# Kernel tuning notes

Measured on AMD Instinct MI355X. Metric: run time of the kernel, lower is better.

Reference implementation:

```python
import jax, jax.numpy as jnp
import numpy as np

EPS = 1e-5


def setup_inputs() -> dict:
    key = jax.random.key(0)
    ks = jax.random.split(key, 4)
    b, c, h, w = 4, 256, 64, 64
    x = jax.random.normal(ks[0], (b, c, h, w), dtype=jnp.float32)
    W_qkv = jax.random.normal(ks[1], (3 * c, c), dtype=jnp.float32) * (1.0 / np.sqrt(c))
    b_qkv = jnp.zeros((3 * c,), dtype=jnp.float32)
    W_out = jax.random.normal(ks[2], (c, c), dtype=jnp.float32) * (1.0 / np.sqrt(c))
    b_out = jnp.zeros((c,), dtype=jnp.float32)
    gamma = jnp.ones((c,), dtype=jnp.float32)
    beta = jnp.zeros((c,), dtype=jnp.float32)
    return {"x": x, "W_qkv": W_qkv, "b_qkv": b_qkv, "W_out": W_out,
            "b_out": b_out, "gamma": gamma, "beta": beta}


def reference(x, W_qkv, b_qkv, W_out, b_out, gamma, beta):
    b, c, h, w = x.shape
    n = h * w  # number of spatial tokens

    # BatchNorm2d (training mode: batch statistics over b,h,w per channel)
    mean = jnp.mean(x, axis=(0, 2, 3), keepdims=True)
    var = jnp.var(x, axis=(0, 2, 3), keepdims=True)
    x_norm = (x - mean) * jax.lax.rsqrt(var + EPS)
    x_norm = x_norm * gamma[None, :, None, None] + beta[None, :, None, None]

    # 1x1 conv to QKV: [b, 3c, h, w]
    qkv = jnp.einsum('bchw,oc->bohw', x_norm, W_qkv) + b_qkv[None, :, None, None]
    q, k, v = jnp.split(qkv, 3, axis=1)

    q = q.transpose(0, 2, 3, 1).reshape(b, n, c)  # [b, n, c]
    k = k.reshape(b, c, n)                         # [b, c, n]
    v = v.transpose(0, 2, 3, 1).reshape(b, n, c)  # [b, n, c]

    scale = c ** (-0.5)
    dot = jnp.einsum('bqc,bck->bqk', q, k) * scale  # [b, n, n]
    attn = jax.nn.softmax(dot, axis=-1)
    out = jnp.einsum('bqk,bkc->bqc', attn, v)       # [b, n, c]
    out = out.reshape(b, h, w, c).transpose(0, 3, 1, 2)  # [b, c, h, w]

    # 1x1 output conv + residual
    out = jnp.einsum('bchw,oc->bohw', out, W_out) + b_out[None, :, None, None]
    return out + x
```

## Files before the change

kernel.cpp:

```cpp
#include <hip/hip_runtime.h>
#include <hip/hip_bf16.h>

typedef __attribute__((ext_vector_type(4))) float f32x4;
typedef __attribute__((ext_vector_type(8))) short bf16x8;
typedef __attribute__((ext_vector_type(4))) unsigned int u32x4;

#define BB 4
#define C 256
#define N 4096
#define TS 32
#define EPSI 1e-5f

__device__ __forceinline__ unsigned short f2bf(float f) {
    unsigned int u = __builtin_bit_cast(unsigned int, f);
    u += 0x7fffu + ((u >> 16) & 1u);
    return (unsigned short)(u >> 16);
}

__device__ __forceinline__ float bf2f(unsigned short h) {
    unsigned int u = ((unsigned int)h) << 16;
    return __builtin_bit_cast(float, u);
}

__device__ __forceinline__ unsigned int cvt_pk_bf16(float lo, float hi) {
    unsigned int r;
    asm("v_cvt_pk_bf16_f32 %0, %1, %2" : "=v"(r) : "v"(lo), "v"(hi));
    return r;
}

__device__ __forceinline__ void stage16(const unsigned short* g, unsigned short* l) {
    __builtin_amdgcn_global_load_lds(
        (const __attribute__((address_space(1))) void*)g,
        (__attribute__((address_space(3))) void*)l, 16, 0, 0);
}

__global__ __launch_bounds__(256) void bn_stats_k(
    const float* __restrict__ x, const float* __restrict__ gamma,
    const float* __restrict__ beta, float* __restrict__ scale, float* __restrict__ shift)
{
    int c = blockIdx.x;
    int tid = threadIdx.x;
    float s = 0.f, s2 = 0.f;
    for (int b = 0; b < BB; ++b) {
        const float4* p = (const float4*)(x + ((size_t)b * C + c) * N);
        for (int i = tid; i < N / 4; i += 256) {
            float4 v = p[i];
            s  += v.x + v.y + v.z + v.w;
            s2 += v.x * v.x + v.y * v.y + v.z * v.z + v.w * v.w;
        }
    }
    for (int m = 1; m < 64; m <<= 1) {
        s  += __shfl_xor(s, m);
        s2 += __shfl_xor(s2, m);
    }
    __shared__ float rs[4], rs2[4];
    int w = tid >> 6;
    if ((tid & 63) == 0) { rs[w] = s; rs2[w] = s2; }
    __syncthreads();
    if (tid == 0) {
        float S  = rs[0] + rs[1] + rs[2] + rs[3];
        float S2 = rs2[0] + rs2[1] + rs2[2] + rs2[3];
        const float inv_n = 1.f / (BB * N);
        float mean = S * inv_n;
        float var  = S2 * inv_n - mean * mean;
        float sc = gamma[c] * rsqrtf(var + EPSI);
        scale[c] = sc;
        shift[c] = beta[c] - mean * sc;
    }
}

__global__ __launch_bounds__(256) void qkv_gemm_k(
    const float* __restrict__ x, const float* __restrict__ Wqkv, const float* __restrict__ bqkv,
    const float* __restrict__ scale, const float* __restrict__ shift,
    unsigned short* __restrict__ q, unsigned short* __restrict__ kt, unsigned short* __restrict__ v)
{
    __shared__ unsigned short Alds[128 * 40];
    __shared__ unsigned short Blds[64 * 40];
    int tid = threadIdx.x;
    int b  = blockIdx.z;
    int T0 = blockIdx.y * 128;
    int O0 = blockIdx.x * 64;
    int lane = tid & 63;
    int w = tid >> 6;
    int wm = w >> 1, wn = w & 1;
    int g = lane >> 4, l15 = lane & 15;

    f32x4 acc[4][2];
    for (int i = 0; i < 4; ++i)
        for (int j = 0; j < 2; ++j) acc[i][j] = f32x4{0.f, 0.f, 0.f, 0.f};

    int a_c = tid >> 3;
    int a_t = (tid & 7) * 16;
    int b_o = tid >> 2;
    int b_c = (tid & 3) * 8;

    for (int c0 = 0; c0 < C; c0 += 32) {
        {
            int cg = c0 + a_c;
            const float4* xp = (const float4*)(x + ((size_t)b * C + cg) * N + T0 + a_t);
            float sc = scale[cg], sh = shift[cg];
            for (int j = 0; j < 4; ++j) {
                float4 vv = xp[j];
                int t = a_t + j * 4;
                Alds[(t + 0) * 40 + a_c] = f2bf(vv.x * sc + sh);
                Alds[(t + 1) * 40 + a_c] = f2bf(vv.y * sc + sh);
                Alds[(t + 2) * 40 + a_c] = f2bf(vv.z * sc + sh);
                Alds[(t + 3) * 40 + a_c] = f2bf(vv.w * sc + sh);
            }
        }
        {
            const float4* wp = (const float4*)(Wqkv + (size_t)(O0 + b_o) * C + c0 + b_c);
            float4 v0 = wp[0], v1 = wp[1];
            int base = b_o * 40 + b_c;
            Blds[base + 0] = f2bf(v0.x); Blds[base + 1] = f2bf(v0.y);
            Blds[base + 2] = f2bf(v0.z); Blds[base + 3] = f2bf(v0.w);
            Blds[base + 4] = f2bf(v1.x); Blds[base + 5] = f2bf(v1.y);
            Blds[base + 6] = f2bf(v1.z); Blds[base + 7] = f2bf(v1.w);
        }
        __syncthreads();
        bf16x8 bfr[2];
        for (int nf = 0; nf < 2; ++nf)
            bfr[nf] = *(const bf16x8*)&Blds[(wn * 32 + nf * 16 + l15) * 40 + g * 8];
        for (int mf = 0; mf < 4; ++mf) {
            bf16x8 afr = *(const bf16x8*)&Alds[(wm * 64 + mf * 16 + l15) * 40 + g * 8];
            for (int nf = 0; nf < 2; ++nf)
                acc[mf][nf] = __builtin_amdgcn_mfma_f32_16x16x32_bf16(afr, bfr[nf], acc[mf][nf], 0, 0, 0);
        }
        __syncthreads();
    }
    const float QSCALE = 0.0625f * 1.44269504088896f;
    for (int mf = 0; mf < 4; ++mf) {
        for (int nf = 0; nf < 2; ++nf) {
            int o = O0 + wn * 32 + nf * 16 + l15;
            float bias = bqkv[o];
            for (int r = 0; r < 4; ++r) {
                int t = T0 + wm * 64 + mf * 16 + g * 4 + r;
                float val = acc[mf][nf][r] + bias;
                if (O0 < 256) {
                    q[((size_t)b * N + t) * C + o] = f2bf(val * QSCALE);
                } else if (O0 < 512) {
                    kt[((size_t)b * N + t) * C + (o - 256)] = f2bf(val);
                } else {
                    int tp = (t & ~31) | ((g * 2 + (mf & 1)) * 4 + r);
                    v[((size_t)b * C + (o - 512)) * N + tp] = f2bf(val);
                }
            }
        }
    }
}

template<int NSEG>
__global__ __launch_bounds__(256, 2) void attn_k(
    const unsigned short* __restrict__ q, const unsigned short* __restrict__ kt,
    const unsigned short* __restrict__ v,
    unsigned short* __restrict__ P, float* __restrict__ ml)
{
    constexpr int NS  = N / NSEG;
    constexpr int NIT = NS / TS;
    __shared__ unsigned short Klds[2][TS * 256];
    __shared__ unsigned short Vlds[2][256 * TS];

    int tid = threadIdx.x;
    int h  = blockIdx.y;
    int b  = blockIdx.z;
    int Q0 = blockIdx.x * 128;
    int lane = tid & 63;
    int lw = tid >> 6;
    int g = lane >> 4, l15 = lane & 15;

    bf16x8 qf[2][8];
#pragma unroll
    for (int m = 0; m < 2; ++m) {
        const unsigned short* qp = q + ((size_t)b * N + Q0 + lw * 32 + m * 16 + l15) * C + g * 8;
#pragma unroll
        for (int kc = 0; kc < 8; ++kc)
            qf[m][kc] = *(const bf16x8*)(qp + kc * 32);
    }

    f32x4 oacc[2][16];
#pragma unroll
    for (int m = 0; m < 2; ++m)
#pragma unroll
        for (int i = 0; i < 16; ++i) oacc[m][i] = f32x4{0.f, 0.f, 0.f, 0.f};
    float mrow[2] = {-1e30f, -1e30f}, lrow[2] = {0.f, 0.f};

    const unsigned short* kb = kt + ((size_t)b * N + h * NS) * C;
    const unsigned short* vb = v + (size_t)b * C * N + h * NS;

#define STAGE(buf_, t_)                                                              \
    {                                                                                \
        const unsigned short* kbt = kb + (size_t)(t_) * TS * 256;                    \
        _Pragma("unroll")                                                            \
        for (int j = 0; j < 4; ++j) {                                                \
            int qq = tid + j * 256;                                                  \
            int tk = qq >> 5, sc = qq & 31;                                          \
            stage16(kbt + tk * 256 + ((sc ^ (tk & 7)) * 8), &Klds[buf_][qq * 8]);    \
        }                                                                            \
        _Pragma("unroll")                                                            \
        for (int j = 0; j < 4; ++j) {                                                \
            int qq = tid + j * 256;                                                  \
            int c = qq >> 2, sl = qq & 3;                                            \
            stage16(vb + (size_t)c * N + (t_) * TS + ((sl ^ ((c >> 1) & 3)) * 8),    \
                    &Vlds[buf_][qq * 8]);                                            \
        }                                                                            \
    }

    STAGE(0, 0);
    __syncthreads();

    for (int t = 0; t < NIT; ++t) {
        int cur = t & 1;
        if (t < NIT - 1) STAGE(cur ^ 1, t + 1);

        f32x4 st[2][2];
#pragma unroll
        for (int m = 0; m < 2; ++m)
#pragma unroll
            for (int ct = 0; ct < 2; ++ct) st[m][ct] = f32x4{0.f, 0.f, 0.f, 0.f};
        __builtin_amdgcn_s_setprio(1);
#pragma unroll
        for (int kc = 0; kc < 8; ++kc) {
#pragma unroll
            for (int ct = 0; ct < 2; ++ct) {
                int tk = ct * 16 + l15;
                int slot = (kc * 4 + g) ^ (tk & 7);
                bf16x8 kf = *(const bf16x8*)&Klds[cur][tk * 256 + slot * 8];
                st[0][ct] = __builtin_amdgcn_mfma_f32_16x16x32_bf16(kf, qf[0][kc], st[0][ct], 0, 0, 0);
                st[1][ct] = __builtin_amdgcn_mfma_f32_16x16x32_bf16(kf, qf[1][kc], st[1][ct], 0, 0, 0);
            }
        }
        __builtin_amdgcn_s_setprio(0);

        float mx[2];
#pragma unroll
        for (int m = 0; m < 2; ++m) {
            float v0 = fmaxf(fmaxf(fmaxf(st[m][0][0], st[m][0][1]), fmaxf(st[m][0][2], st[m][0][3])),
                             fmaxf(fmaxf(st[m][1][0], st[m][1][1]), fmaxf(st[m][1][2], st[m][1][3])));
            v0 = fmaxf(v0, __shfl_xor(v0, 16));
            v0 = fmaxf(v0, __shfl_xor(v0, 32));
            mx[m] = v0;
        }
        bool ok = (mx[0] - mrow[0] <= 8.f) & (mx[1] - mrow[1] <= 8.f);
        if (!__all(ok)) {
#pragma unroll
            for (int m = 0; m < 2; ++m) {
                float mn = fmaxf(mrow[m], mx[m]);
                float alpha = exp2f(mrow[m] - mn);
                mrow[m] = mn;
                lrow[m] *= alpha;
#pragma unroll
                for (int f = 0; f < 16; ++f)
#pragma unroll
                    for (int r = 0; r < 4; ++r) oacc[m][f][r] *= alpha;
            }
        }
        bf16x8 pf[2];
#pragma unroll
        for (int m = 0; m < 2; ++m) {
            float rs = 0.f;
#pragma unroll
            for (int ct = 0; ct < 2; ++ct)
#pragma unroll
                for (int r = 0; r < 4; ++r) {
                    float p = exp2f(st[m][ct][r] - mrow[m]);
                    st[m][ct][r] = p;
                    rs += p;
                }
            rs += __shfl_xor(rs, 16);
            rs += __shfl_xor(rs, 32);
            lrow[m] += rs;
            u32x4 pk;
            pk[0] = cvt_pk_bf16(st[m][0][0], st[m][0][1]);
            pk[1] = cvt_pk_bf16(st[m][0][2], st[m][0][3]);
            pk[2] = cvt_pk_bf16(st[m][1][0], st[m][1][1]);
            pk[3] = cvt_pk_bf16(st[m][1][2], st[m][1][3]);
            pf[m] = __builtin_bit_cast(bf16x8, pk);
        }

        __builtin_amdgcn_s_setprio(1);
#pragma unroll
        for (int cf = 0; cf < 16; ++cf) {
            int c = cf * 16 + l15;
            int vslot = g ^ ((c >> 1) & 3);
            bf16x8 vf = *(const bf16x8*)&Vlds[cur][c * TS + vslot * 8];
            oacc[0][cf] = __builtin_amdgcn_mfma_f32_16x16x32_bf16(vf, pf[0], oacc[0][cf], 0, 0, 0);
            oacc[1][cf] = __builtin_amdgcn_mfma_f32_16x16x32_bf16(vf, pf[1], oacc[1][cf], 0, 0, 0);
        }
        __builtin_amdgcn_s_setprio(0);
        __syncthreads();
    }

#pragma unroll
    for (int m = 0; m < 2; ++m) {
        size_t tokid = (size_t)b * N + Q0 + lw * 32 + m * 16 + l15;
        if (g == 0) {
            ml[(size_t)(2 * h + 0) * (BB * N) + tokid] = mrow[m];
            ml[(size_t)(2 * h + 1) * (BB * N) + tokid] = lrow[m];
        }
        unsigned short* pp = P + (size_t)h * BB * N * C + tokid * C;
#pragma unroll
        for (int cf = 0; cf < 16; ++cf) {
#pragma unroll
            for (int rp = 0; rp < 2; ++rp) {
                int c = cf * 16 + g * 4 + rp * 2;
                unsigned int pk2 = cvt_pk_bf16(oacc[m][cf][rp * 2 + 0], oacc[m][cf][rp * 2 + 1]);
                *(unsigned int*)&pp[c] = pk2;
            }
        }
    }
}

template<int NSEG>
__global__ __launch_bounds__(256) void out_gemm_k(
    const unsigned short* __restrict__ P, const float* __restrict__ ml,
    const float* __restrict__ Wout, const float* __restrict__ bout,
    const float* __restrict__ x, float* __restrict__ out)
{
    __shared__ unsigned short Alds[64 * 72];
    __shared__ unsigned short Blds[128 * 72];
    int tid = threadIdx.x;
    int b   = blockIdx.z;
    int CO0 = blockIdx.y * 64;
    int T0  = blockIdx.x * 128;
    int lane = tid & 63;
    int w = tid >> 6;
    int wm = w >> 1, wn = w & 1;
    int g = lane >> 4, l15 = lane & 15;

    f32x4 acc[2][4];
    for (int i = 0; i < 2; ++i)
        for (int j = 0; j < 4; ++j) acc[i][j] = f32x4{0.f, 0.f, 0.f, 0.f};

    int a_r = tid >> 2;
    int a_cb = (tid & 3) * 16;

    float cw[4][NSEG];
    float cinv[4];
#pragma unroll
    for (int it = 0; it < 4; ++it) {
        int tl = (tid + it * 256) >> 3;
        size_t tok = (size_t)b * N + T0 + tl;
        float ms[NSEG], ls[NSEG];
#pragma unroll
        for (int s = 0; s < NSEG; ++s) {
            ms[s] = ml[(size_t)(2 * s + 0) * (BB * N) + tok];
            ls[s] = ml[(size_t)(2 * s + 1) * (BB * N) + tok];
        }
        float M = ms[0];
#pragma unroll
        for (int s = 1; s < NSEG; ++s) M = fmaxf(M, ms[s]);
        float den = 0.f;
#pragma unroll
        for (int s = 0; s < NSEG; ++s) {
            cw[it][s] = exp2f(ms[s] - M);
            den += cw[it][s] * ls[s];
        }
        cinv[it] = 1.f / den;
    }

    for (int c0 = 0; c0 < C; c0 += 64) {
        {
            const float4* wp = (const float4*)(Wout + (size_t)(CO0 + a_r) * C + c0 + a_cb);
            for (int j = 0; j < 4; ++j) {
                float4 vv = wp[j];
                int base = a_r * 72 + a_cb + j * 4;
                Alds[base + 0] = f2bf(vv.x);
                Alds[base + 1] = f2bf(vv.y);
                Alds[base + 2] = f2bf(vv.z);
                Alds[base + 3] = f2bf(vv.w);
            }
        }
#pragma unroll
        for (int it = 0; it < 4; ++it) {
            int chunk = tid + it * 256;
            int tl = chunk >> 3, j = chunk & 7;
            size_t base = ((size_t)b * N + T0 + tl) * C + c0 + j * 8;
            float val[8];
#pragma unroll
            for (int e = 0; e < 8; ++e) val[e] = 0.f;
#pragma unroll
            for (int s = 0; s < NSEG; ++s) {
                bf16x8 p = *(const bf16x8*)(P + (size_t)s * BB * N * C + base);
                float wgt = cw[it][s];
#pragma unroll
                for (int e = 0; e < 8; ++e) val[e] += wgt * bf2f((unsigned short)p[e]);
            }
            unsigned int opk[4];
#pragma unroll
            for (int jj = 0; jj < 4; ++jj)
                opk[jj] = cvt_pk_bf16(val[2 * jj] * cinv[it], val[2 * jj + 1] * cinv[it]);
            *(u32x4*)&Blds[tl * 72 + j * 8] = *(u32x4*)opk;
        }
        __syncthreads();
        for (int kk = 0; kk < 2; ++kk) {
            bf16x8 bfr[4];
            for (int nf = 0; nf < 4; ++nf)
                bfr[nf] = *(const bf16x8*)&Blds[(wn * 64 + nf * 16 + l15) * 72 + kk * 32 + g * 8];
            for (int mf = 0; mf < 2; ++mf) {
                bf16x8 afr = *(const bf16x8*)&Alds[(wm * 32 + mf * 16 + l15) * 72 + kk * 32 + g * 8];
                for (int nf = 0; nf < 4; ++nf)
                    acc[mf][nf] = __builtin_amdgcn_mfma_f32_16x16x32_bf16(afr, bfr[nf], acc[mf][nf], 0, 0, 0);
            }
        }
        __syncthreads();
    }
    for (int mf = 0; mf < 2; ++mf) {
        for (int nf = 0; nf < 4; ++nf) {
            int t = T0 + wn * 64 + nf * 16 + l15;
            for (int r = 0; r < 4; ++r) {
                int co = CO0 + wm * 32 + mf * 16 + g * 4 + r;
                size_t oidx = ((size_t)b * C + co) * N + t;
                out[oidx] = acc[mf][nf][r] + bout[co] + x[oidx];
            }
        }
    }
}

extern "C" void kernel_launch(void* const* d_in, const int* in_sizes, int n_in,
                              void* d_out, int out_size, void* d_ws, size_t ws_size,
                              hipStream_t stream) {
    const float* x     = (const float*)d_in[0];
    const float* Wqkv  = (const float*)d_in[1];
    const float* bqkv  = (const float*)d_in[2];
    const float* Wout  = (const float*)d_in[3];
    const float* bout  = (const float*)d_in[4];
    const float* gamma = (const float*)d_in[5];
    const float* beta  = (const float*)d_in[6];
    float* out = (float*)d_out;

    const size_t BBNC = (size_t)BB * N * C;
    char* ws = (char*)d_ws;
    float* scale = (float*)ws;
    float* shift = (float*)(ws + 1024);
    unsigned short* q  = (unsigned short*)(ws + 4096);
    unsigned short* kt = q  + BBNC;
    unsigned short* v  = kt + BBNC;
    unsigned short* P  = v  + BBNC;

    size_t need4 = 4096 + 7 * BBNC * 2 + (size_t)8 * BB * N * 4;

    bn_stats_k<<<dim3(C), dim3(256), 0, stream>>>(x, gamma, beta, scale, shift);
    qkv_gemm_k<<<dim3(12, 32, BB), dim3(256), 0, stream>>>(x, Wqkv, bqkv, scale, shift, q, kt, v);

    if (ws_size >= need4) {
        float* ml = (float*)(P + 4 * BBNC);
        attn_k<4><<<dim3(N / 128, 4, BB), dim3(256), 0, stream>>>(q, kt, v, P, ml);
        out_gemm_k<4><<<dim3(32, 4, BB), dim3(256), 0, stream>>>(P, ml, Wout, bout, x, out);
    } else {
        float* ml = (float*)(P + 2 * BBNC);
        attn_k<2><<<dim3(N / 128, 2, BB), dim3(256), 0, stream>>>(q, kt, v, P, ml);
        out_gemm_k<2><<<dim3(32, 4, BB), dim3(256), 0, stream>>>(P, ml, Wout, bout, x, out);
    }
}
```

Before: 171.1 us.

## Restructure QKV and output GEMMs around token tiles, pre-convert Wqkv to bf16

A new pre-pass converts Wqkv to bf16 once. The QKV GEMM now normalizes a 32-token tile of x across all channels a single time, then loops over all 12 output-channel blocks, staging the bf16 weights into swizzled LDS with direct global-to-LDS loads. Previously each of the 12 output blocks re-read and re-normalized x. The output GEMM likewise moves to 32-token tiles that cover all 256 output channels, so each token's combined P segments are merged once instead of once per output-channel block. The cost is smaller token tiles, more weight traffic per block, and an extra kernel launch.

Measured after the change: 152.5 us. 10.8% less time.

```diff
diff --git a/kernel.cpp b/kernel.cpp
--- a/kernel.cpp
+++ b/kernel.cpp
@@ -11,6 +11,8 @@
 #define TS 32
 #define EPSI 1e-5f
 
+constexpr size_t BBNC = (size_t)BB * N * C;
+
 __device__ __forceinline__ unsigned short f2bf(float f) {
     unsigned int u = __builtin_bit_cast(unsigned int, f);
     u += 0x7fffu + ((u >> 16) & 1u);
@@ -32,6 +34,20 @@
     __builtin_amdgcn_global_load_lds(
         (const __attribute__((address_space(1))) void*)g,
         (__attribute__((address_space(3))) void*)l, 16, 0, 0);
+}
+
+__global__ __launch_bounds__(256) void w2bf_k(const float* __restrict__ W,
+                                              unsigned short* __restrict__ wb)
+{
+    size_t i = (size_t)blockIdx.x * 256 + threadIdx.x;
+    const float4* p = (const float4*)(W + i * 8);
+    float4 a = p[0], c = p[1];
+    unsigned int pk[4];
+    pk[0] = cvt_pk_bf16(a.x, a.y);
+    pk[1] = cvt_pk_bf16(a.z, a.w);
+    pk[2] = cvt_pk_bf16(c.x, c.y);
+    pk[3] = cvt_pk_bf16(c.z, c.w);
+    *(u32x4*)(wb + i * 8) = *(u32x4*)pk;
 }
 
 __global__ __launch_bounds__(256) void bn_stats_k(
@@ -70,78 +86,86 @@
 }
 
 __global__ __launch_bounds__(256) void qkv_gemm_k(
-    const float* __restrict__ x, const float* __restrict__ Wqkv, const float* __restrict__ bqkv,
+    const float* __restrict__ x, const unsigned short* __restrict__ wqkv_bf,
+    const float* __restrict__ bqkv,
     const float* __restrict__ scale, const float* __restrict__ shift,
     unsigned short* __restrict__ q, unsigned short* __restrict__ kt, unsigned short* __restrict__ v)
 {
-    __shared__ unsigned short Alds[128 * 40];
-    __shared__ unsigned short Blds[64 * 40];
+    __shared__ unsigned short Alds[32 * 264];
+    __shared__ unsigned short Wlds[64 * 256];
+
     int tid = threadIdx.x;
-    int b  = blockIdx.z;
-    int T0 = blockIdx.y * 128;
-    int O0 = blockIdx.x * 64;
+    int b  = blockIdx.y;
+    int T0 = blockIdx.x * 32;
     int lane = tid & 63;
     int w = tid >> 6;
     int wm = w >> 1, wn = w & 1;
     int g = lane >> 4, l15 = lane & 15;
 
-    f32x4 acc[4][2];
-    for (int i = 0; i < 4; ++i)
-        for (int j = 0; j < 2; ++j) acc[i][j] = f32x4{0.f, 0.f, 0.f, 0.f};
-
-    int a_c = tid >> 3;
-    int a_t = (tid & 7) * 16;
-    int b_o = tid >> 2;
-    int b_c = (tid & 3) * 8;
-
-    for (int c0 = 0; c0 < C; c0 += 32) {
-        {
-            int cg = c0 + a_c;
-            const float4* xp = (const float4*)(x + ((size_t)b * C + cg) * N + T0 + a_t);
-            float sc = scale[cg], sh = shift[cg];
+    {
+        int cbase = tid >> 1;
+        int t0 = (tid & 1) * 16;
+#pragma unroll
+        for (int pass = 0; pass < 2; ++pass) {
+            int cc = cbase + pass * 128;
+            const float4* xp = (const float4*)(x + ((size_t)b * C + cc) * N + T0 + t0);
+            float sc = scale[cc], sh = shift[cc];
+#pragma unroll
             for (int j = 0; j < 4; ++j) {
                 float4 vv = xp[j];
-                int t = a_t + j * 4;
-                Alds[(t + 0) * 40 + a_c] = f2bf(vv.x * sc + sh);
-                Alds[(t + 1) * 40 + a_c] = f2bf(vv.y * sc + sh);
-                Alds[(t + 2) * 40 + a_c] = f2bf(vv.z * sc + sh);
-                Alds[(t + 3) * 40 + a_c] = f2bf(vv.w * sc + sh);
-            }
-        }
+                int t = t0 + j * 4;
+                Alds[(t + 0) * 264 + cc] = f2bf(vv.x * sc + sh);
+                Alds[(t + 1) * 264 + cc] = f2bf(vv.y * sc + sh);
+                Alds[(t + 2) * 264 + cc] = f2bf(vv.z * sc + sh);
+                Alds[(t + 3) * 264 + cc] = f2bf(vv.w * sc + sh);
+            }
+        }
+    }
+
+    const float QSCALE = 0.0625f * 1.44269504088896f;
+
+    for (int oi = 0; oi < 12; ++oi) {
+        int O0 = oi * 64;
+        __syncthreads();
         {
-            const float4* wp = (const float4*)(Wqkv + (size_t)(O0 + b_o) * C + c0 + b_c);
-            float4 v0 = wp[0], v1 = wp[1];
-            int base = b_o * 40 + b_c;
-            Blds[base + 0] = f2bf(v0.x); Blds[base + 1] = f2bf(v0.y);
-            Blds[base + 2] = f2bf(v0.z); Blds[base + 3] = f2bf(v0.w);
-            Blds[base + 4] = f2bf(v1.x); Blds[base + 5] = f2bf(v1.y);
-            Blds[base + 6] = f2bf(v1.z); Blds[base + 7] = f2bf(v1.w);
+            const unsigned short* wb = wqkv_bf + (size_t)O0 * 256;
+#pragma unroll
+            for (int j = 0; j < 8; ++j) {
+                int qq = tid + j * 256;
+                int lo = qq >> 5, sc2 = qq & 31;
+                stage16(wb + (size_t)lo * 256 + ((sc2 ^ (lo & 7)) * 8), &Wlds[qq * 8]);
+            }
         }
         __syncthreads();
-        bf16x8 bfr[2];
-        for (int nf = 0; nf < 2; ++nf)
-            bfr[nf] = *(const bf16x8*)&Blds[(wn * 32 + nf * 16 + l15) * 40 + g * 8];
-        for (int mf = 0; mf < 4; ++mf) {
-            bf16x8 afr = *(const bf16x8*)&Alds[(wm * 64 + mf * 16 + l15) * 40 + g * 8];
-            for (int nf = 0; nf < 2; ++nf)
-                acc[mf][nf] = __builtin_amdgcn_mfma_f32_16x16x32_bf16(afr, bfr[nf], acc[mf][nf], 0, 0, 0);
-        }
-        __syncthreads();
-    }
-    const float QSCALE = 0.0625f * 1.44269504088896f;
-    for (int mf = 0; mf < 4; ++mf) {
+
+        f32x4 acc[2];
+        acc[0] = f32x4{0.f, 0.f, 0.f, 0.f};
+        acc[1] = f32x4{0.f, 0.f, 0.f, 0.f};
+#pragma unroll
+        for (int kk = 0; kk < 8; ++kk) {
+            bf16x8 afr = *(const bf16x8*)&Alds[(wm * 16 + l15) * 264 + kk * 32 + g * 8];
+#pragma unroll
+            for (int nf = 0; nf < 2; ++nf) {
+                int lo = wn * 32 + nf * 16 + l15;
+                bf16x8 bfr = *(const bf16x8*)&Wlds[lo * 256 + (((kk * 4 + g) ^ (lo & 7)) * 8)];
+                acc[nf] = __builtin_amdgcn_mfma_f32_16x16x32_bf16(afr, bfr, acc[nf], 0, 0, 0);
+            }
+        }
+
+#pragma unroll
         for (int nf = 0; nf < 2; ++nf) {
             int o = O0 + wn * 32 + nf * 16 + l15;
             float bias = bqkv[o];
+#pragma unroll
             for (int r = 0; r < 4; ++r) {
-                int t = T0 + wm * 64 + mf * 16 + g * 4 + r;
-                float val = acc[mf][nf][r] + bias;
+                int t = T0 + wm * 16 + g * 4 + r;
+                float val = acc[nf][r] + bias;
                 if (O0 < 256) {
                     q[((size_t)b * N + t) * C + o] = f2bf(val * QSCALE);
                 } else if (O0 < 512) {
                     kt[((size_t)b * N + t) * C + (o - 256)] = f2bf(val);
                 } else {
-                    int tp = (t & ~31) | ((g * 2 + (mf & 1)) * 4 + r);
+                    int tp = (t & ~31) | ((g * 2 + wm) * 4 + r);
                     v[((size_t)b * C + (o - 512)) * N + tp] = f2bf(val);
                 }
             }
@@ -297,7 +321,7 @@
             ml[(size_t)(2 * h + 0) * (BB * N) + tokid] = mrow[m];
             ml[(size_t)(2 * h + 1) * (BB * N) + tokid] = lrow[m];
         }
-        unsigned short* pp = P + (size_t)h * BB * N * C + tokid * C;
+        unsigned short* pp = P + (size_t)h * BBNC + tokid * C;
 #pragma unroll
         for (int cf = 0; cf < 16; ++cf) {
 #pragma unroll
@@ -316,29 +340,19 @@
     const float* __restrict__ Wout, const float* __restrict__ bout,
     const float* __restrict__ x, float* __restrict__ out)
 {
-    __shared__ unsigned short Alds[64 * 72];
-    __shared__ unsigned short Blds[128 * 72];
+    __shared__ unsigned short Alds[256 * 40];
+    __shared__ unsigned short Blds[32 * 40];
+
     int tid = threadIdx.x;
-    int b   = blockIdx.z;
-    int CO0 = blockIdx.y * 64;
-    int T0  = blockIdx.x * 128;
+    int b  = blockIdx.y;
+    int T0 = blockIdx.x * 32;
     int lane = tid & 63;
     int w = tid >> 6;
-    int wm = w >> 1, wn = w & 1;
     int g = lane >> 4, l15 = lane & 15;
 
-    f32x4 acc[2][4];
-    for (int i = 0; i < 2; ++i)
-        for (int j = 0; j < 4; ++j) acc[i][j] = f32x4{0.f, 0.f, 0.f, 0.f};
-
-    int a_r = tid >> 2;
-    int a_cb = (tid & 3) * 16;
-
-    float cw[4][NSEG];
-    float cinv[4];
-#pragma unroll
-    for (int it = 0; it < 4; ++it) {
-        int tl = (tid + it * 256) >> 3;
+    int tl = (tid >> 2) & 31;
+    float cw[NSEG], cinv;
+    {
         size_t tok = (size_t)b * N + T0 + tl;
         float ms[NSEG], ls[NSEG];
 #pragma unroll
@@ -352,65 +366,77 @@
         float den = 0.f;
 #pragma unroll
         for (int s = 0; s < NSEG; ++s) {
-            cw[it][s] = exp2f(ms[s] - M);
-            den += cw[it][s] * ls[s];
-        }
-        cinv[it] = 1.f / den;
-    }
-
-    for (int c0 = 0; c0 < C; c0 += 64) {
+            cw[s] = exp2f(ms[s] - M);
+            den += cw[s] * ls[s];
+        }
+        cinv = 1.f / den;
+    }
+
+    f32x4 acc[4][2];
+#pragma unroll
+    for (int i = 0; i < 4; ++i)
+#pragma unroll
+        for (int j = 0; j < 2; ++j) acc[i][j] = f32x4{0.f, 0.f, 0.f, 0.f};
+
+    for (int c0 = 0; c0 < C; c0 += 32) {
+        if (c0) __syncthreads();
         {
-            const float4* wp = (const float4*)(Wout + (size_t)(CO0 + a_r) * C + c0 + a_cb);
-            for (int j = 0; j < 4; ++j) {
+            const float4* wp = (const float4*)(Wout + (size_t)tid * C + c0);
+            unsigned int wpk[16];
+#pragma unroll
+            for (int j = 0; j < 8; ++j) {
                 float4 vv = wp[j];
-                int base = a_r * 72 + a_cb + j * 4;
-                Alds[base + 0] = f2bf(vv.x);
-                Alds[base + 1] = f2bf(vv.y);
-                Alds[base + 2] = f2bf(vv.z);
-                Alds[base + 3] = f2bf(vv.w);
-            }
-        }
-#pragma unroll
-        for (int it = 0; it < 4; ++it) {
-            int chunk = tid + it * 256;
-            int tl = chunk >> 3, j = chunk & 7;
+                wpk[2 * j + 0] = cvt_pk_bf16(vv.x, vv.y);
+                wpk[2 * j + 1] = cvt_pk_bf16(vv.z, vv.w);
+            }
+#pragma unroll
+            for (int j = 0; j < 16; ++j)
+                *(unsigned int*)&Alds[tid * 40 + j * 2] = wpk[j];
+        }
+        if (tid < 128) {
+            int j = tid & 3;
             size_t base = ((size_t)b * N + T0 + tl) * C + c0 + j * 8;
             float val[8];
 #pragma unroll
             for (int e = 0; e < 8; ++e) val[e] = 0.f;
 #pragma unroll
             for (int s = 0; s < NSEG; ++s) {
-                bf16x8 p = *(const bf16x8*)(P + (size_t)s * BB * N * C + base);
-                float wgt = cw[it][s];
+                bf16x8 p = *(const bf16x8*)(P + (size_t)s * BBNC + base);
+                float wgt = cw[s];
 #pragma unroll
                 for (int e = 0; e < 8; ++e) val[e] += wgt * bf2f((unsigned short)p[e]);
             }
             unsigned int opk[4];
 #pragma unroll
             for (int jj = 0; jj < 4; ++jj)
-                opk[jj] = cvt_pk_bf16(val[2 * jj] * cinv[it], val[2 * jj + 1] * cinv[it]);
-            *(u32x4*)&Blds[tl * 72 + j * 8] = *(u32x4*)opk;
+                opk[jj] = cvt_pk_bf16(val[2 * jj] * cinv, val[2 * jj + 1] * cinv);
+            *(u32x4*)&Blds[tl * 40 + j * 8] = *(u32x4*)opk;
         }
         __syncthreads();
-        for (int kk = 0; kk < 2; ++kk) {
-            bf16x8 bfr[4];
-            for (int nf = 0; nf < 4; ++nf)
-                bfr[nf] = *(const bf16x8*)&Blds[(wn * 64 + nf * 16 + l15) * 72 + kk * 32 + g * 8];
-            for (int mf = 0; mf < 2; ++mf) {
-                bf16x8 afr = *(const bf16x8*)&Alds[(wm * 32 + mf * 16 + l15) * 72 + kk * 32 + g * 8];
-                for (int nf = 0; nf < 4; ++nf)
-                    acc[mf][nf] = __builtin_amdgcn_mfma_f32_16x16x32_bf16(afr, bfr[nf], acc[mf][nf], 0, 0, 0);
-            }
-        }
-        __syncthreads();
-    }
-    for (int mf = 0; mf < 2; ++mf) {
-        for (int nf = 0; nf < 4; ++nf) {
-            int t = T0 + wn * 64 + nf * 16 + l15;
+
+        bf16x8 afr[4];
+#pragma unroll
+        for (int mf = 0; mf < 4; ++mf)
+            afr[mf] = *(const bf16x8*)&Alds[(w * 64 + mf * 16 + l15) * 40 + g * 8];
+#pragma unroll
+        for (int tf = 0; tf < 2; ++tf) {
+            bf16x8 bfr = *(const bf16x8*)&Blds[(tf * 16 + l15) * 40 + g * 8];
+#pragma unroll
+            for (int mf = 0; mf < 4; ++mf)
+                acc[mf][tf] = __builtin_amdgcn_mfma_f32_16x16x32_bf16(afr[mf], bfr, acc[mf][tf], 0, 0, 0);
+        }
+    }
+
+#pragma unroll
+    for (int mf = 0; mf < 4; ++mf) {
+#pragma unroll
+        for (int tf = 0; tf < 2; ++tf) {
+            int t = T0 + tf * 16 + l15;
+#pragma unroll
             for (int r = 0; r < 4; ++r) {
-                int co = CO0 + wm * 32 + mf * 16 + g * 4 + r;
+                int co = w * 64 + mf * 16 + g * 4 + r;
                 size_t oidx = ((size_t)b * C + co) * N + t;
-                out[oidx] = acc[mf][nf][r] + bout[co] + x[oidx];
+                out[oidx] = acc[mf][tf][r] + bout[co] + x[oidx];
             }
         }
     }
@@ -428,7 +454,6 @@
     const float* beta  = (const float*)d_in[6];
     float* out = (float*)d_out;
 
-    const size_t BBNC = (size_t)BB * N * C;
     char* ws = (char*)d_ws;
     float* scale = (float*)ws;
     float* shift = (float*)(ws + 1024);
@@ -436,19 +461,21 @@
     unsigned short* kt = q  + BBNC;
     unsigned short* v  = kt + BBNC;
     unsigned short* P  = v  + BBNC;
+    unsigned short* wqkv_bf = P;
 
     size_t need4 = 4096 + 7 * BBNC * 2 + (size_t)8 * BB * N * 4;
 
+    w2bf_k<<<dim3(768 * 256 / 8 / 256), dim3(256), 0, stream>>>(Wqkv, wqkv_bf);
     bn_stats_k<<<dim3(C), dim3(256), 0, stream>>>(x, gamma, beta, scale, shift);
-    qkv_gemm_k<<<dim3(12, 32, BB), dim3(256), 0, stream>>>(x, Wqkv, bqkv, scale, shift, q, kt, v);
+    qkv_gemm_k<<<dim3(N / 32, BB), dim3(256), 0, stream>>>(x, wqkv_bf, bqkv, scale, shift, q, kt, v);
 
     if (ws_size >= need4) {
         float* ml = (float*)(P + 4 * BBNC);
         attn_k<4><<<dim3(N / 128, 4, BB), dim3(256), 0, stream>>>(q, kt, v, P, ml);
-        out_gemm_k<4><<<dim3(32, 4, BB), dim3(256), 0, stream>>>(P, ml, Wout, bout, x, out);
+        out_gemm_k<4><<<dim3(N / 32, BB), dim3(256), 0, stream>>>(P, ml, Wout, bout, x, out);
     } else {
         float* ml = (float*)(P + 2 * BBNC);
         attn_k<2><<<dim3(N / 128, 2, BB), dim3(256), 0, stream>>>(q, kt, v, P, ml);
-        out_gemm_k<2><<<dim3(32, 4, BB), dim3(256), 0, stream>>>(P, ml, Wout, bout, x, out);
-    }
-}
+        out_gemm_k<2><<<dim3(N / 32, BB), dim3(256), 0, stream>>>(P, ml, Wout, bout, x, out);
+    }
+}
```
